# Kernel tuning notes

Measured on AMD Instinct MI355X. Metric: run time of the kernel, lower is better.

The kernel has to match this reference:

```python
import jax, jax.numpy as jnp
from jax import lax
import numpy as np

B, T, C, H = 1024, 256, 6, 32  # batch, time, channels (6 LSTMs), hidden
G = 4 * H  # gate dim (i,f,g,o), PyTorch order


def setup_inputs() -> dict:
    key = jax.random.key(0)
    ks = jax.random.split(key, 12)
    s = 1.0 / np.sqrt(H)  # PyTorch LSTM/Linear init scale
    u = lambda k, shape, sc: jax.random.uniform(k, shape, jnp.float32, -sc, sc)
    x = jax.random.normal(ks[0], (B, T, C), jnp.float32)
    # 6 channel-wise LSTMs stacked on leading axis (input_size=1 -> w_ih is [C, G])
    w_ih = u(ks[1], (C, G), s)
    w_hh = u(ks[2], (C, G, H), s)
    b_ih = u(ks[3], (C, G), s)
    b_hh = u(ks[4], (C, G), s)
    # MLP head: fc1 (192->64), fc3 (64->64), fc2 (64->2), PyTorch Linear layout [out,in]
    s1 = 1.0 / np.sqrt(C * H)
    w1 = u(ks[5], (64, C * H), s1); b1 = u(ks[6], (64,), s1)
    s3 = 1.0 / np.sqrt(64)
    w3 = u(ks[7], (64, 64), s3); b3 = u(ks[8], (64,), s3)
    w2 = u(ks[9], (2, 64), s3); b2 = u(ks[10], (2,), s3)
    return {"x": x, "w_ih": w_ih, "w_hh": w_hh, "b_ih": b_ih, "b_hh": b_hh,
            "w1": w1, "b1": b1, "w3": w3, "b3": b3, "w2": w2, "b2": b2}


def _grouped_lstm(x, w_ih, w_hh, b_ih, b_hh):
    # x: [B, T, C]; runs C independent hidden-32 LSTMs fused in one scan.
    b = b_ih + b_hh  # [C, G]

    def step(carry, x_t):
        h, c = carry  # [B, C, H] each
        gates = x_t[:, :, None] * w_ih[None] + jnp.einsum('cgh,bch->bcg', w_hh, h) + b
        i, f, g, o = jnp.split(gates, 4, axis=-1)
        c = jax.nn.sigmoid(f) * c + jax.nn.sigmoid(i) * jnp.tanh(g)
        h = jax.nn.sigmoid(o) * jnp.tanh(c)
        return (h, c), h

    h0 = jnp.zeros((x.shape[0], C, H), x.dtype)
    _, hs = lax.scan(step, (h0, h0), jnp.swapaxes(x, 0, 1))  # hs: [T, B, C, H]
    return jnp.transpose(hs, (1, 0, 2, 3)).reshape(x.shape[0], x.shape[1], C * H)


def reference(x, w_ih, w_hh, b_ih, b_hh, w1, b1, w3, b3, w2, b2):
    x7 = _grouped_lstm(x, w_ih, w_hh, b_ih, b_hh)  # [B, T, 192] == cat of 6 LSTM outputs
    h = jax.nn.relu(x7[:, -1, :] @ w1.T + b1)
    h = jax.nn.relu(h @ w3.T + b3)
    out = h @ w2.T + b2  # [B, 2]
    return (out, x7)
```

## Files before the change

### kernel.cpp

```cpp
#include <hip/hip_runtime.h>
#include <hip/hip_bf16.h>


#define Bv 1024
#define Tv 256
#define Cv 6
#define Hv 32
#define Gv 128

#define L2E 1.442695041f

__global__ __launch_bounds__(256) void lstm_kernel(
    const float* __restrict__ x,
    const float* __restrict__ w_ih,
    const float* __restrict__ w_hh,
    const float* __restrict__ b_ih,
    const float* __restrict__ b_hh,
    float* __restrict__ x7)
{
    __shared__ float hbuf[4][Hv];

    const int wave = threadIdx.x >> 6;
    const int lane = threadIdx.x & 63;
    const int c    = blockIdx.x % Cv;
    const int b    = (blockIdx.x / Cv) * 4 + wave;

    float w0[Hv], w1r[Hv];
    const float* whc = w_hh + (size_t)c * (Gv * Hv);
    #pragma unroll
    for (int j4 = 0; j4 < Hv / 4; ++j4) {
        float4 a = *(const float4*)(whc + lane * Hv + j4 * 4);
        float4 q = *(const float4*)(whc + (lane + 64) * Hv + j4 * 4);
        w0[j4*4+0] = a.x; w0[j4*4+1] = a.y; w0[j4*4+2] = a.z; w0[j4*4+3] = a.w;
        w1r[j4*4+0] = q.x; w1r[j4*4+1] = q.y; w1r[j4*4+2] = q.z; w1r[j4*4+3] = q.w;
    }
    const float wi0 = w_ih[c * Gv + lane];
    const float wi1 = w_ih[c * Gv + lane + 64];
    const float bb0 = b_ih[c * Gv + lane] + b_hh[c * Gv + lane];
    const float bb1 = b_ih[c * Gv + lane + 64] + b_hh[c * Gv + lane + 64];

    const bool  lo   = (lane < 32);
    const float nsc1 = lo ? (-2.0f * L2E) : (-L2E);
    const float fa   = lo ? 2.0f : 1.0f;
    const float fb   = lo ? -1.0f : 0.0f;

    if (lane < Hv) hbuf[wave][lane] = 0.0f;
    float cc = 0.0f;

    const float* xp = x + (size_t)b * Tv * Cv + c;
    float* op = x7 + (size_t)b * Tv * (Cv * Hv) + c * Hv + (lane & 31);

    float xt = xp[0];
    for (int t = 0; t < Tv; ++t) {
        float xn = (t + 1 < Tv) ? xp[(size_t)(t + 1) * Cv] : 0.0f;

        float g0a = fmaf(xt, wi0, bb0), g0b = 0.0f;
        float g1a = fmaf(xt, wi1, bb1), g1b = 0.0f;
        const float4* hb4 = (const float4*)hbuf[wave];
        #pragma unroll
        for (int j4 = 0; j4 < Hv / 4; ++j4) {
            float4 h4 = hb4[j4];
            g0a += w0[j4*4+0] * h4.x;  g1a += w1r[j4*4+0] * h4.x;
            g0b += w0[j4*4+1] * h4.y;  g1b += w1r[j4*4+1] * h4.y;
            g0a += w0[j4*4+2] * h4.z;  g1a += w1r[j4*4+2] * h4.z;
            g0b += w0[j4*4+3] * h4.w;  g1b += w1r[j4*4+3] * h4.w;
        }
        float g0 = g0a + g0b;
        float g1 = g1a + g1b;

        float e0 = __builtin_amdgcn_exp2f(g0 * -L2E);
        float s0 = __builtin_amdgcn_rcpf(1.0f + e0);
        float e1 = __builtin_amdgcn_exp2f(g1 * nsc1);
        float u1 = __builtin_amdgcn_rcpf(1.0f + e1);
        float to = fmaf(u1, fa, fb);

        float f_s = __shfl_xor(s0, 32);
        float o_s = __shfl_xor(to, 32);

        cc = fmaf(f_s, cc, s0 * to);
        float e2 = __builtin_amdgcn_exp2f(cc * (-2.0f * L2E));
        float u2 = __builtin_amdgcn_rcpf(1.0f + e2);
        float th = fmaf(u2, 2.0f, -1.0f);
        float hn = o_s * th;

        if (lane < Hv) {
            hbuf[wave][lane] = hn;
            op[(size_t)t * (Cv * Hv)] = hn;
        }
        xt = xn;
    }
}

__global__ __launch_bounds__(64) void head_kernel(
    const float* __restrict__ x7,
    const float* __restrict__ w1, const float* __restrict__ b1,
    const float* __restrict__ w3, const float* __restrict__ b3,
    const float* __restrict__ w2, const float* __restrict__ b2,
    float* __restrict__ out)
{
    const int b   = blockIdx.x;
    const int tid = threadIdx.x;
    __shared__ float xr[Cv * Hv];
    __shared__ float h1[64];
    __shared__ float h2[64];

    const float* xrow = x7 + ((size_t)b * Tv + (Tv - 1)) * (Cv * Hv);
    if (tid < 48) ((float4*)xr)[tid] = ((const float4*)xrow)[tid];
    __syncthreads();

    float acc[4] = {0.f, 0.f, 0.f, 0.f};
    const float4* w4 = (const float4*)(w1 + tid * (Cv * Hv));
    const float4* x4 = (const float4*)xr;
    #pragma unroll
    for (int k = 0; k < 48; ++k) {
        float4 w = w4[k], xv = x4[k];
        acc[k & 3] += (w.x * xv.x + w.y * xv.y) + (w.z * xv.z + w.w * xv.w);
    }
    h1[tid] = fmaxf((acc[0] + acc[1]) + (acc[2] + acc[3]) + b1[tid], 0.0f);
    __syncthreads();

    float bcc[4] = {0.f, 0.f, 0.f, 0.f};
    const float4* w34 = (const float4*)(w3 + tid * 64);
    const float4* h14 = (const float4*)h1;
    #pragma unroll
    for (int k = 0; k < 16; ++k) {
        float4 w = w34[k], hv = h14[k];
        bcc[k & 3] += (w.x * hv.x + w.y * hv.y) + (w.z * hv.z + w.w * hv.w);
    }
    h2[tid] = fmaxf((bcc[0] + bcc[1]) + (bcc[2] + bcc[3]) + b3[tid], 0.0f);
    __syncthreads();

    if (tid < 2) {
        float a2 = b2[tid];
        const float* w2r = w2 + tid * 64;
        #pragma unroll 4
        for (int k = 0; k < 64; ++k) a2 += w2r[k] * h2[k];
        out[b * 2 + tid] = a2;
    }
}

extern "C" void kernel_launch(void* const* d_in, const int* in_sizes, int n_in,
                              void* d_out, int out_size, void* d_ws, size_t ws_size,
                              hipStream_t stream) {
    const float* x    = (const float*)d_in[0];
    const float* w_ih = (const float*)d_in[1];
    const float* w_hh = (const float*)d_in[2];
    const float* b_ih = (const float*)d_in[3];
    const float* b_hh = (const float*)d_in[4];
    const float* w1   = (const float*)d_in[5];
    const float* b1   = (const float*)d_in[6];
    const float* w3   = (const float*)d_in[7];
    const float* b3   = (const float*)d_in[8];
    const float* w2   = (const float*)d_in[9];
    const float* b2   = (const float*)d_in[10];

    float* out = (float*)d_out;
    float* x7  = out + (size_t)Bv * 2;

    lstm_kernel<<<dim3((Bv / 4) * Cv), dim3(256), 0, stream>>>(x, w_ih, w_hh, b_ih, b_hh, x7);
    head_kernel<<<dim3(Bv), dim3(64), 0, stream>>>(x7, w1, b1, w3, b3, w2, b2, out);
}
```

Baseline: 456.5 us.

## Compute LSTM recurrent matmul with fp16 MFMA over 16-batch tiles

Replaces the per-lane scalar FMA dot products, one batch element per wave, with 16x16x32 fp16 MFMA instructions. Each block now processes 16 batch rows of one channel, and two waves split the hidden units. The hidden state is double-buffered in LDS as fp16 and each timestep ends with a block barrier. The aim is to cut recurrent-matmul ALU work per step and reuse the weights across 16 batch rows. In exchange, the recurrent weights and hidden state are quantised to fp16, which lowers precision, and the grid shrinks to 384 blocks of 128 threads, which may leave the GPU underoccupied.

Result: faster. 395.4 us (-13.4%).

```diff
diff --git a/kernel.cpp b/kernel.cpp
--- a/kernel.cpp
+++ b/kernel.cpp
@@ -10,7 +10,18 @@
 
 #define L2E 1.442695041f
 
-__global__ __launch_bounds__(256) void lstm_kernel(
+typedef _Float16 f16x8 __attribute__((ext_vector_type(8)));
+typedef float f32x4v __attribute__((ext_vector_type(4)));
+
+__device__ __forceinline__ float fsig(float v) {
+    return __builtin_amdgcn_rcpf(1.0f + __builtin_amdgcn_exp2f(v * -L2E));
+}
+__device__ __forceinline__ float ftanh2(float v) {
+    float u = __builtin_amdgcn_rcpf(1.0f + __builtin_amdgcn_exp2f(v * (-2.0f * L2E)));
+    return fmaf(u, 2.0f, -1.0f);
+}
+
+__global__ __launch_bounds__(128) void lstm_kernel(
     const float* __restrict__ x,
     const float* __restrict__ w_ih,
     const float* __restrict__ w_hh,
@@ -18,75 +29,92 @@
     const float* __restrict__ b_hh,
     float* __restrict__ x7)
 {
-    __shared__ float hbuf[4][Hv];
+    __shared__ _Float16 hlds[2][16][40];
 
-    const int wave = threadIdx.x >> 6;
-    const int lane = threadIdx.x & 63;
-    const int c    = blockIdx.x % Cv;
-    const int b    = (blockIdx.x / Cv) * 4 + wave;
+    const int tid  = threadIdx.x;
+    const int wv   = tid >> 6;
+    const int lane = tid & 63;
+    const int r16  = lane & 15;
+    const int grp  = lane >> 4;
 
-    float w0[Hv], w1r[Hv];
+    const int c  = blockIdx.x % Cv;
+    const int nb = (blockIdx.x / Cv) * 16;
+
+    {
+        _Float16* hz = &hlds[0][0][0];
+        for (int i = tid; i < 2 * 16 * 40; i += 128) hz[i] = (_Float16)0.0f;
+    }
+
     const float* whc = w_hh + (size_t)c * (Gv * Hv);
+    f16x8 afrag[4];
     #pragma unroll
-    for (int j4 = 0; j4 < Hv / 4; ++j4) {
-        float4 a = *(const float4*)(whc + lane * Hv + j4 * 4);
-        float4 q = *(const float4*)(whc + (lane + 64) * Hv + j4 * 4);
-        w0[j4*4+0] = a.x; w0[j4*4+1] = a.y; w0[j4*4+2] = a.z; w0[j4*4+3] = a.w;
-        w1r[j4*4+0] = q.x; w1r[j4*4+1] = q.y; w1r[j4*4+2] = q.z; w1r[j4*4+3] = q.w;
+    for (int q = 0; q < 4; ++q) {
+        const float* wr = whc + (q * 32 + wv * 16 + r16) * Hv + grp * 8;
+        float4 wa = *(const float4*)(wr);
+        float4 wb = *(const float4*)(wr + 4);
+        f16x8 a;
+        a[0] = (_Float16)wa.x; a[1] = (_Float16)wa.y;
+        a[2] = (_Float16)wa.z; a[3] = (_Float16)wa.w;
+        a[4] = (_Float16)wb.x; a[5] = (_Float16)wb.y;
+        a[6] = (_Float16)wb.z; a[7] = (_Float16)wb.w;
+        afrag[q] = a;
     }
-    const float wi0 = w_ih[c * Gv + lane];
-    const float wi1 = w_ih[c * Gv + lane + 64];
-    const float bb0 = b_ih[c * Gv + lane] + b_hh[c * Gv + lane];
-    const float bb1 = b_ih[c * Gv + lane + 64] + b_hh[c * Gv + lane + 64];
+    float4 bias4[4], wih4[4];
+    #pragma unroll
+    for (int q = 0; q < 4; ++q) {
+        const int rb = q * 32 + wv * 16 + grp * 4;
+        float4 bi = *(const float4*)(b_ih + c * Gv + rb);
+        float4 bh = *(const float4*)(b_hh + c * Gv + rb);
+        bias4[q] = make_float4(bi.x + bh.x, bi.y + bh.y, bi.z + bh.z, bi.w + bh.w);
+        wih4[q]  = *(const float4*)(w_ih + c * Gv + rb);
+    }
 
-    const bool  lo   = (lane < 32);
-    const float nsc1 = lo ? (-2.0f * L2E) : (-L2E);
-    const float fa   = lo ? 2.0f : 1.0f;
-    const float fb   = lo ? -1.0f : 0.0f;
+    float cst[4] = {0.0f, 0.0f, 0.0f, 0.0f};
+    const float* xp = x + ((size_t)(nb + r16) * Tv) * Cv + c;
+    float* op = x7 + ((size_t)(nb + r16) * Tv) * (Cv * Hv) + c * Hv + wv * 16 + grp * 4;
 
-    if (lane < Hv) hbuf[wave][lane] = 0.0f;
-    float cc = 0.0f;
-
-    const float* xp = x + (size_t)b * Tv * Cv + c;
-    float* op = x7 + (size_t)b * Tv * (Cv * Hv) + c * Hv + (lane & 31);
+    __syncthreads();
 
     float xt = xp[0];
+    int p = 0;
     for (int t = 0; t < Tv; ++t) {
-        float xn = (t + 1 < Tv) ? xp[(size_t)(t + 1) * Cv] : 0.0f;
+        int tn = (t + 1 < Tv) ? (t + 1) : (Tv - 1);
+        float xn = xp[tn * Cv];
 
-        float g0a = fmaf(xt, wi0, bb0), g0b = 0.0f;
-        float g1a = fmaf(xt, wi1, bb1), g1b = 0.0f;
-        const float4* hb4 = (const float4*)hbuf[wave];
+        f16x8 bfrag = *(const f16x8*)(&hlds[p][r16][grp * 8]);
+
+        f32x4v acc[4];
         #pragma unroll
-        for (int j4 = 0; j4 < Hv / 4; ++j4) {
-            float4 h4 = hb4[j4];
-            g0a += w0[j4*4+0] * h4.x;  g1a += w1r[j4*4+0] * h4.x;
-            g0b += w0[j4*4+1] * h4.y;  g1b += w1r[j4*4+1] * h4.y;
-            g0a += w0[j4*4+2] * h4.z;  g1a += w1r[j4*4+2] * h4.z;
-            g0b += w0[j4*4+3] * h4.w;  g1b += w1r[j4*4+3] * h4.w;
+        for (int q = 0; q < 4; ++q) {
+            acc[q][0] = fmaf(xt, wih4[q].x, bias4[q].x);
+            acc[q][1] = fmaf(xt, wih4[q].y, bias4[q].y);
+            acc[q][2] = fmaf(xt, wih4[q].z, bias4[q].z);
+            acc[q][3] = fmaf(xt, wih4[q].w, bias4[q].w);
+            acc[q] = __builtin_amdgcn_mfma_f32_16x16x32_f16(afrag[q], bfrag, acc[q], 0, 0, 0);
         }
-        float g0 = g0a + g0b;
-        float g1 = g1a + g1b;
 
-        float e0 = __builtin_amdgcn_exp2f(g0 * -L2E);
-        float s0 = __builtin_amdgcn_rcpf(1.0f + e0);
-        float e1 = __builtin_amdgcn_exp2f(g1 * nsc1);
-        float u1 = __builtin_amdgcn_rcpf(1.0f + e1);
-        float to = fmaf(u1, fa, fb);
+        float h4[4];
+        #pragma unroll
+        for (int r = 0; r < 4; ++r) {
+            float i_s = fsig(acc[0][r]);
+            float f_s = fsig(acc[1][r]);
+            float g_t = ftanh2(acc[2][r]);
+            float o_s = fsig(acc[3][r]);
+            float cr  = fmaf(f_s, cst[r], i_s * g_t);
+            cst[r] = cr;
+            h4[r] = o_s * ftanh2(cr);
+        }
 
-        float f_s = __shfl_xor(s0, 32);
-        float o_s = __shfl_xor(to, 32);
+        *(float4*)(op + (size_t)t * (Cv * Hv)) = make_float4(h4[0], h4[1], h4[2], h4[3]);
 
-        cc = fmaf(f_s, cc, s0 * to);
-        float e2 = __builtin_amdgcn_exp2f(cc * (-2.0f * L2E));
-        float u2 = __builtin_amdgcn_rcpf(1.0f + e2);
-        float th = fmaf(u2, 2.0f, -1.0f);
-        float hn = o_s * th;
+        auto pk0 = __builtin_amdgcn_cvt_pkrtz(h4[0], h4[1]);
+        auto pk1 = __builtin_amdgcn_cvt_pkrtz(h4[2], h4[3]);
+        uint2 pk = make_uint2(__builtin_bit_cast(unsigned int, pk0),
+                              __builtin_bit_cast(unsigned int, pk1));
+        *(uint2*)(&hlds[p ^ 1][r16][wv * 16 + grp * 4]) = pk;
 
-        if (lane < Hv) {
-            hbuf[wave][lane] = hn;
-            op[(size_t)t * (Cv * Hv)] = hn;
-        }
+        __syncthreads();
+        p ^= 1;
         xt = xn;
     }
 }
@@ -102,7 +130,7 @@
     const int tid = threadIdx.x;
     __shared__ float xr[Cv * Hv];
     __shared__ float h1[64];
-    __shared__ float h2[64];
+    __shared__ float h2s[64];
 
     const float* xrow = x7 + ((size_t)b * Tv + (Tv - 1)) * (Cv * Hv);
     if (tid < 48) ((float4*)xr)[tid] = ((const float4*)xrow)[tid];
@@ -127,14 +155,14 @@
         float4 w = w34[k], hv = h14[k];
         bcc[k & 3] += (w.x * hv.x + w.y * hv.y) + (w.z * hv.z + w.w * hv.w);
     }
-    h2[tid] = fmaxf((bcc[0] + bcc[1]) + (bcc[2] + bcc[3]) + b3[tid], 0.0f);
+    h2s[tid] = fmaxf((bcc[0] + bcc[1]) + (bcc[2] + bcc[3]) + b3[tid], 0.0f);
     __syncthreads();
 
     if (tid < 2) {
         float a2 = b2[tid];
         const float* w2r = w2 + tid * 64;
         #pragma unroll 4
-        for (int k = 0; k < 64; ++k) a2 += w2r[k] * h2[k];
+        for (int k = 0; k < 64; ++k) a2 += w2r[k] * h2s[k];
         out[b * 2 + tid] = a2;
     }
 }
@@ -157,6 +185,6 @@
     float* out = (float*)d_out;
     float* x7  = out + (size_t)Bv * 2;
 
-    lstm_kernel<<<dim3((Bv / 4) * Cv), dim3(256), 0, stream>>>(x, w_ih, w_hh, b_ih, b_hh, x7);
+    lstm_kernel<<<dim3((Bv / 16) * Cv), dim3(128), 0, stream>>>(x, w_ih, w_hh, b_ih, b_hh, x7);
     head_kernel<<<dim3(Bv), dim3(64), 0, stream>>>(x7, w1, b1, w3, b3, w2, b2, out);
 }
```
